# Kernel optimization log

Hardware: AMD Instinct MI355X
Metric: run time of the kernel (lower is better)

## Reference

```python
import jax, jax.numpy as jnp
import numpy as np

B, SEQ, DIM = 32, 512, 1024
DEPTH, HEADS, DHEAD = 6, 8, 64
INNER = HEADS * DHEAD  # 512
NLAT, MAXSEQ = 64, 512
EPS = 1e-5


def setup_inputs() -> dict:
    key = jax.random.key(0)
    ks = jax.random.split(key, 8)
    return {
        "x": jax.random.normal(ks[0], (B, SEQ, DIM), dtype=jnp.float32),
        "attention_mask": jax.random.randint(ks[1], (B, SEQ), 0, 2, dtype=jnp.int32),
        "latents": jax.random.normal(ks[2], (NLAT, DIM), dtype=jnp.float32),
        "media_pos_emb": jax.random.normal(ks[3], (MAXSEQ, DIM), dtype=jnp.float32),
        "ln_media_g": jnp.ones((DEPTH, DIM), jnp.float32),
        "ln_media_b": jnp.zeros((DEPTH, DIM), jnp.float32),
        "ln_lat_g": jnp.ones((DEPTH, DIM), jnp.float32),
        "ln_lat_b": jnp.zeros((DEPTH, DIM), jnp.float32),
        "Wq": jax.random.normal(ks[4], (DEPTH, DIM, INNER), dtype=jnp.float32) * 0.02,
        "Wkv": jax.random.normal(ks[5], (DEPTH, DIM, 2 * INNER), dtype=jnp.float32) * 0.02,
        "Wout": jax.random.normal(ks[6], (DEPTH, INNER, DIM), dtype=jnp.float32) * 0.02,
        "final_g": jnp.ones((DIM,), jnp.float32),
        "final_b": jnp.zeros((DIM,), jnp.float32),
    }


def _layer_norm(x, g, b):
    mu = jnp.mean(x, axis=-1, keepdims=True)
    var = jnp.mean(jnp.square(x - mu), axis=-1, keepdims=True)
    return (x - mu) * jax.lax.rsqrt(var + EPS) * g + b


def _heads(t):
    # b n (h d) -> b h n d
    b, n, _ = t.shape
    return t.reshape(b, n, HEADS, DHEAD).transpose(0, 2, 1, 3)


def reference(x, attention_mask, latents, media_pos_emb, ln_media_g, ln_media_b,
              ln_lat_g, ln_lat_b, Wq, Wkv, Wout, final_g, final_b):
    b, seq, _ = x.shape
    x = x + media_pos_emb[None, :seq, :]
    lat = jnp.broadcast_to(latents[None], (b, NLAT, DIM))
    scale = DHEAD ** -0.5
    # key mask over [latents ++ media]: latent keys never masked; 1 == masked
    key_mask = jnp.concatenate(
        [jnp.zeros((b, NLAT), attention_mask.dtype), attention_mask], axis=1)
    masked = (key_mask == 1)[:, None, None, :]  # b 1 1 j
    for l in range(DEPTH):
        xm = _layer_norm(x, ln_media_g[l], ln_media_b[l])
        ln = _layer_norm(lat, ln_lat_g[l], ln_lat_b[l])
        q = _heads(ln @ Wq[l])                      # b h i d
        kv = jnp.concatenate([ln, xm], axis=1) @ Wkv[l]
        k, v = jnp.split(kv, 2, axis=-1)
        k, v = _heads(k), _heads(v)                 # b h j d
        sim = jnp.einsum('bhid,bhjd->bhij', q * scale, k)
        sim = jnp.where(masked, -jnp.inf, sim)
        attn = jax.nn.softmax(sim, axis=-1)
        out = jnp.einsum('bhij,bhjd->bhid', attn, v)
        out = out.transpose(0, 2, 1, 3).reshape(b, NLAT, INNER)
        lat = lat + out @ Wout[l]
    return _layer_norm(lat, final_g, final_b)
```

## Files before the change

kernel.cpp:

```cpp
#include <hip/hip_runtime.h>
#include <cstdint>


#define DEVINL __device__ __forceinline__

typedef __attribute__((ext_vector_type(8))) short short8_t;
typedef __attribute__((ext_vector_type(4))) float f32x4;

DEVINL ushort f2bf(float f) {
  union { float f; uint32_t u; } c; c.f = f;
  uint32_t u = c.u;
  u += ((u >> 16) & 1u) + 0x7fffu;
  return (ushort)(u >> 16);
}
DEVINL float bf2f(ushort u) {
  union { uint32_t u; float f; } c; c.u = ((uint32_t)u) << 16;
  return c.f;
}
DEVINL f32x4 mfma16(short8_t a, short8_t b, f32x4 c) {
  return __builtin_amdgcn_mfma_f32_16x16x32_bf16(a, b, c, 0, 0, 0);
}
DEVINL void gld16(ushort* lds, const ushort* g) {
  __builtin_amdgcn_global_load_lds(
      (const __attribute__((address_space(1))) void*)g,
      (__attribute__((address_space(3))) void*)lds, 16, 0, 0);
}

__global__ __launch_bounds__(512, 2) void k_gemm256m(const ushort* __restrict__ A,
    const ushort* __restrict__ Bt, const float* __restrict__ bias,
    ushort* __restrict__ Kb, ushort* __restrict__ Vt) {
  extern __shared__ char lds[];
  constexpr int K = 1024, NT = 16;
  int tid = threadIdx.x, lane = tid & 63, w = tid >> 6;
  int wm = w >> 2, wn = w & 3;
  int fr = lane & 15;
  int fkb = (lane >> 4) << 4;
  int xorv = (fr & 7) << 4;
  int bid = blockIdx.x;
  int xcd = bid & 7, ii = bid >> 3;
  int m0 = (xcd * 8 + (ii >> 2)) * 256;
  int n0 = (ii & 3) * 256;
  int srow = w * 8 + (lane >> 3);
  int sce = ((lane & 7) ^ (lane >> 3)) << 3;
  const ushort* Ag = A + (size_t)(m0 + srow) * K + sce;
  const ushort* Bg = Bt + (size_t)(n0 + srow) * K + sce;
  f32x4 acc[8][4] = {};

  auto stA = [&](int t, int h) {
    ushort* d = (ushort*)(lds + (t % 3) * 32768 + h * 16384 + w * 1024);
    const ushort* s = Ag + (size_t)(h * 128) * K + t * 64;
    gld16(d, s);
    gld16((ushort*)((char*)d + 8192), s + (size_t)64 * K);
  };
  auto stB = [&](int t, int h) {
    ushort* d = (ushort*)(lds + 98304 + (t & 1) * 32768 + h * 16384 + w * 1024);
    const ushort* s = Bg + (size_t)(h * 128) * K + t * 64;
    gld16(d, s);
    gld16((ushort*)((char*)d + 8192), s + (size_t)64 * K);
  };
  stA(0, 0); stA(0, 1); stB(0, 0); stB(0, 1); stA(1, 0); stA(1, 1);

#define PHASE(MQ, STAGE_STMT)                                                  \
  do {                                                                         \
    _Pragma("unroll") for (int m2 = 0; m2 < 2; ++m2)                           \
      _Pragma("unroll") for (int kh = 0; kh < 2; ++kh)                         \
        afr[m2][kh] = *(const short8_t*)(ab +                                  \
            ((wm * 128 + (MQ + m2) * 16 + fr) << 7) +                          \
            ((kh * 64 + fkb) ^ xorv));                                         \
    STAGE_STMT;                                                                \
    asm volatile("s_waitcnt lgkmcnt(0)" ::: "memory");                         \
    __builtin_amdgcn_s_setprio(1);                                             \
    _Pragma("unroll") for (int m2 = 0; m2 < 2; ++m2)                           \
      _Pragma("unroll") for (int nt = 0; nt < 4; ++nt)                         \
        _Pragma("unroll") for (int kh = 0; kh < 2; ++kh)                       \
          acc[MQ + m2][nt] = mfma16(afr[m2][kh], bfr[nt][kh], acc[MQ + m2][nt]); \
    __builtin_amdgcn_s_setprio(0);                                             \
    __builtin_amdgcn_s_barrier();                                              \
  } while (0)

  for (int t = 0; t < NT; ++t) {
    const char* ab = lds + (t % 3) * 32768;
    const char* bb = lds + 98304 + (t & 1) * 32768;
    short8_t bfr[4][2], afr[2][2];
    if (t + 1 < NT) asm volatile("s_waitcnt vmcnt(4)" ::: "memory");
    else            asm volatile("s_waitcnt vmcnt(0)" ::: "memory");
    __builtin_amdgcn_s_barrier();
#pragma unroll
    for (int nt = 0; nt < 4; ++nt)
#pragma unroll
      for (int kh = 0; kh < 2; ++kh)
        bfr[nt][kh] = *(const short8_t*)(bb +
            ((wn * 64 + nt * 16 + fr) << 7) + ((kh * 64 + fkb) ^ xorv));
    PHASE(0, { if (t + 1 < NT) stB(t + 1, 0); });
    PHASE(2, { if (t + 1 < NT) stB(t + 1, 1); });
    PHASE(4, { if (t + 2 < NT) stA(t + 2, 0); });
    PHASE(6, { if (t + 2 < NT) stA(t + 2, 1); });
  }
#undef PHASE

  __syncthreads();
  ushort* Cl = (ushort*)lds;
  constexpr int CLS = 264;
  for (int p = 0; p < 2; ++p) {
    if (p) __syncthreads();
    if (wm == p) {
#pragma unroll
      for (int mt = 0; mt < 8; ++mt)
#pragma unroll
        for (int nt = 0; nt < 4; ++nt)
#pragma unroll
          for (int r = 0; r < 4; ++r) {
            int rl = mt * 16 + ((lane >> 4) << 2) + r;
            int cl = wn * 64 + nt * 16 + (lane & 15);
            Cl[rl * CLS + cl] = f2bf(acc[mt][nt][r] + bias[n0 + cl]);
          }
    }
    __syncthreads();
    int rowg0 = m0 + p * 128;
    int b_ = rowg0 >> 9;
    int jbase = 64 + (rowg0 & 511);
    if (n0 < 512) {
#pragma unroll
      for (int q2 = 0; q2 < 8; ++q2) {
        int task = tid + q2 * 512;
        int rl = task >> 5, ck = task & 31;
        short8_t vv = *(const short8_t*)&Cl[rl * CLS + ck * 8];
        *(short8_t*)&Kb[((size_t)(b_ * 576 + jbase + rl) << 9) + n0 + ck * 8] = vv;
      }
    } else {
#pragma unroll
      for (int q2 = 0; q2 < 8; ++q2) {
        int task = tid + q2 * 512;
        int d = task >> 4, jg = task & 15;
        short8_t vv;
#pragma unroll
        for (int e = 0; e < 8; ++e) vv[e] = (short)Cl[(jg * 8 + e) * CLS + d];
        *(short8_t*)&Vt[((size_t)(b_ * 512 + (n0 - 512) + d)) * 576 +
                        jbase + jg * 8] = vv;
      }
    }
  }
}

__global__ __launch_bounds__(256) void k_fold_kv(const float* __restrict__ Wkv,
    const float* __restrict__ lnmg, const float* __restrict__ lnlg,
    ushort* __restrict__ wkvmT, ushort* __restrict__ wlatT) {
  __shared__ float tile[32][33];
  int l = blockIdx.z;
  const float* Wl = Wkv + (size_t)l * 1048576;
  int r0 = blockIdx.y * 32, c0 = blockIdx.x * 32;
  int tx = threadIdx.x & 31, ty = threadIdx.x >> 5;
#pragma unroll
  for (int i = 0; i < 4; ++i)
    tile[ty + i * 8][tx] = Wl[(size_t)(r0 + ty + i * 8) * 1024 + c0 + tx];
  __syncthreads();
#pragma unroll
  for (int i = 0; i < 4; ++i) {
    int jl = ty + i * 8;
    float wv = tile[tx][jl];
    int r = r0 + tx, c = c0 + jl;
    wkvmT[(size_t)l * 1048576 + (size_t)c * 1024 + r] = f2bf(wv * lnmg[l * 1024 + r]);
    wlatT[(size_t)l * 1572864 + (size_t)(512 + c) * 1024 + r] = f2bf(wv * lnlg[l * 1024 + r]);
  }
}

__global__ __launch_bounds__(256) void k_fold_q(const float* __restrict__ Wq,
    const float* __restrict__ lnlg, ushort* __restrict__ wlatT) {
  __shared__ float tile[32][33];
  int l = blockIdx.z;
  const float* Wl = Wq + (size_t)l * 524288;
  int r0 = blockIdx.y * 32, c0 = blockIdx.x * 32;
  int tx = threadIdx.x & 31, ty = threadIdx.x >> 5;
#pragma unroll
  for (int i = 0; i < 4; ++i)
    tile[ty + i * 8][tx] = Wl[(size_t)(r0 + ty + i * 8) * 512 + c0 + tx];
  __syncthreads();
#pragma unroll
  for (int i = 0; i < 4; ++i) {
    int jl = ty + i * 8;
    int r = r0 + tx, c = c0 + jl;
    wlatT[(size_t)l * 1572864 + (size_t)c * 1024 + r] =
        f2bf(tile[tx][jl] * lnlg[l * 1024 + r] * 0.125f);
  }
}

__global__ __launch_bounds__(256) void k_fold_out(const float* __restrict__ Wout,
    ushort* __restrict__ woutT) {
  __shared__ float tile[32][33];
  int l = blockIdx.z;
  const float* Wl = Wout + (size_t)l * 524288;
  int r0 = blockIdx.y * 32, c0 = blockIdx.x * 32;
  int tx = threadIdx.x & 31, ty = threadIdx.x >> 5;
#pragma unroll
  for (int i = 0; i < 4; ++i)
    tile[ty + i * 8][tx] = Wl[(size_t)(r0 + ty + i * 8) * 1024 + c0 + tx];
  __syncthreads();
#pragma unroll
  for (int i = 0; i < 4; ++i) {
    int jl = ty + i * 8;
    woutT[(size_t)l * 524288 + (size_t)(c0 + jl) * 512 + r0 + tx] = f2bf(tile[tx][jl]);
  }
}

__global__ __launch_bounds__(256) void k_bias(const float* __restrict__ Wkv,
    const float* __restrict__ Wq, const float* __restrict__ lnmb,
    const float* __restrict__ lnlb, float* __restrict__ bkvm,
    float* __restrict__ blat) {
  __shared__ float red[4][64];
  int l = blockIdx.y;
  int c0 = blockIdx.x * 64;
  int tx = threadIdx.x & 63, dg = threadIdx.x >> 6;
  const float* Wsrc; const float* bv; int ld; float scale = 1.0f; float* outp;
  if (c0 < 1024) {
    Wsrc = Wkv + (size_t)l * 1048576 + c0 + tx; bv = lnmb + l * 1024; ld = 1024;
    outp = bkvm + l * 1024 + c0 + tx;
  } else if (c0 < 1536) {
    Wsrc = Wq + (size_t)l * 524288 + (c0 - 1024) + tx; bv = lnlb + l * 1024; ld = 512;
    outp = blat + l * 1536 + (c0 - 1024) + tx; scale = 0.125f;
  } else {
    Wsrc = Wkv + (size_t)l * 1048576 + (c0 - 1536) + tx; bv = lnlb + l * 1024; ld = 1024;
    outp = blat + l * 1536 + 512 + (c0 - 1536) + tx;
  }
  float acc = 0.f;
  for (int d = dg * 256; d < dg * 256 + 256; ++d)
    acc += bv[d] * Wsrc[(size_t)d * ld];
  red[dg][tx] = acc;
  __syncthreads();
  if (dg == 0) *outp = (red[0][tx] + red[1][tx] + red[2][tx] + red[3][tx]) * scale;
}

__global__ __launch_bounds__(256) void k_rownorm(const float* __restrict__ in,
    const float* __restrict__ pos, ushort* __restrict__ out) {
  int row = blockIdx.x, t = threadIdx.x;
  float4 v = *(const float4*)(in + (size_t)row * 1024 + t * 4);
  if (pos) {
    float4 p = *(const float4*)(pos + (size_t)(row & 511) * 1024 + t * 4);
    v.x += p.x; v.y += p.y; v.z += p.z; v.w += p.w;
  }
  float s = v.x + v.y + v.z + v.w;
  float q = v.x * v.x + v.y * v.y + v.z * v.z + v.w * v.w;
#pragma unroll
  for (int off = 32; off; off >>= 1) { s += __shfl_xor(s, off); q += __shfl_xor(q, off); }
  __shared__ float rs[4], rq[4];
  if ((t & 63) == 0) { rs[t >> 6] = s; rq[t >> 6] = q; }
  __syncthreads();
  s = rs[0] + rs[1] + rs[2] + rs[3];
  q = rq[0] + rq[1] + rq[2] + rq[3];
  float mean = s * (1.0f / 1024.0f);
  float var = q * (1.0f / 1024.0f) - mean * mean;
  float rstd = rsqrtf(var + 1e-5f);
  ushort4 o;
  o.x = f2bf((v.x - mean) * rstd);
  o.y = f2bf((v.y - mean) * rstd);
  o.z = f2bf((v.z - mean) * rstd);
  o.w = f2bf((v.w - mean) * rstd);
  *(ushort4*)(out + (size_t)row * 1024 + t * 4) = o;
}

__global__ __launch_bounds__(256) void k_finalln(const float* __restrict__ in,
    const float* __restrict__ g, const float* __restrict__ b, float* __restrict__ out) {
  int row = blockIdx.x, t = threadIdx.x;
  float4 v = *(const float4*)(in + (size_t)row * 1024 + t * 4);
  float s = v.x + v.y + v.z + v.w;
  float q = v.x * v.x + v.y * v.y + v.z * v.z + v.w * v.w;
#pragma unroll
  for (int off = 32; off; off >>= 1) { s += __shfl_xor(s, off); q += __shfl_xor(q, off); }
  __shared__ float rs[4], rq[4];
  if ((t & 63) == 0) { rs[t >> 6] = s; rq[t >> 6] = q; }
  __syncthreads();
  s = rs[0] + rs[1] + rs[2] + rs[3];
  q = rq[0] + rq[1] + rq[2] + rq[3];
  float mean = s * (1.0f / 1024.0f);
  float var = q * (1.0f / 1024.0f) - mean * mean;
  float rstd = rsqrtf(var + 1e-5f);
  float4 g4 = *(const float4*)(g + t * 4);
  float4 b4 = *(const float4*)(b + t * 4);
  float4 o;
  o.x = (v.x - mean) * rstd * g4.x + b4.x;
  o.y = (v.y - mean) * rstd * g4.y + b4.y;
  o.z = (v.z - mean) * rstd * g4.z + b4.z;
  o.w = (v.w - mean) * rstd * g4.w + b4.w;
  *(float4*)(out + (size_t)row * 1024 + t * 4) = o;
}

__global__ __launch_bounds__(256) void k_latinit(const float* __restrict__ latents,
                                                 float* __restrict__ lat) {
  int row = blockIdx.x, t = threadIdx.x;
  *(float4*)(lat + (size_t)row * 1024 + t * 4) =
      *(const float4*)(latents + (size_t)(row & 63) * 1024 + t * 4);
}

template <int MODE>
__global__ __launch_bounds__(256) void k_gemm64(const ushort* __restrict__ A,
    const ushort* __restrict__ Bt, const float* __restrict__ bias,
    ushort* __restrict__ o0, ushort* __restrict__ o1, ushort* __restrict__ o2,
    float* __restrict__ of, int N, int K) {
  __shared__ ushort Al[2][64][32];
  __shared__ ushort Bl[2][64][32];
  __shared__ ushort Cl[64][72];
  int tid = threadIdx.x, lane = tid & 63, w = tid >> 6;
  int wr = w >> 1, wc = w & 1;
  int m0 = blockIdx.y * 64, n0 = blockIdx.x * 64;
  f32x4 acc[2][2] = {};
  const ushort* Ag = A + (size_t)(m0 + w * 16 + (lane >> 2)) * K + (lane & 3) * 8;
  const ushort* Bg = Bt + (size_t)(n0 + w * 16 + (lane >> 2)) * K + (lane & 3) * 8;
  int fr = lane & 15, fk = (lane >> 4) << 3;
  int nt = K >> 5;
  gld16(&Al[0][w * 16][0], Ag);
  gld16(&Bl[0][w * 16][0], Bg);
  __syncthreads();
  for (int t = 0; t < nt; ++t) {
    int cur = t & 1;
    if (t + 1 < nt) {
      int k0 = (t + 1) << 5;
      gld16(&Al[cur ^ 1][w * 16][0], Ag + k0);
      gld16(&Bl[cur ^ 1][w * 16][0], Bg + k0);
    }
    short8_t a[2], b[2];
#pragma unroll
    for (int mt = 0; mt < 2; ++mt)
      a[mt] = *(const short8_t*)&Al[cur][wr * 32 + mt * 16 + fr][fk];
#pragma unroll
    for (int nt2 = 0; nt2 < 2; ++nt2)
      b[nt2] = *(const short8_t*)&Bl[cur][wc * 32 + nt2 * 16 + fr][fk];
#pragma unroll
    for (int mt = 0; mt < 2; ++mt)
#pragma unroll
      for (int nt2 = 0; nt2 < 2; ++nt2)
        acc[mt][nt2] = mfma16(a[mt], b[nt2], acc[mt][nt2]);
    __syncthreads();
  }
  if constexpr (MODE == 3) {
    if (n0 >= 1024) {
#pragma unroll
      for (int mt = 0; mt < 2; ++mt)
#pragma unroll
        for (int nt2 = 0; nt2 < 2; ++nt2)
#pragma unroll
          for (int r = 0; r < 4; ++r) {
            int rl = wr * 32 + mt * 16 + ((lane >> 4) << 2) + r;
            int col = wc * 32 + nt2 * 16 + (lane & 15);
            Cl[rl][col] = f2bf(acc[mt][nt2][r] + bias[n0 + col]);
          }
      __syncthreads();
      int b_ = m0 >> 6;
#pragma unroll
      for (int q = 0; q < 2; ++q) {
        int task = tid + q * 256;
        int jg = task & 7, d = task >> 3;
        short8_t vv;
#pragma unroll
        for (int e = 0; e < 8; ++e) vv[e] = (short)Cl[jg * 8 + e][d];
        *(short8_t*)&o2[((size_t)(b_ * 512 + (n0 - 1024) + d)) * 576 + jg * 8] = vv;
      }
      return;
    }
  }
#pragma unroll
  for (int mt = 0; mt < 2; ++mt)
#pragma unroll
    for (int nt2 = 0; nt2 < 2; ++nt2)
#pragma unroll
      for (int r = 0; r < 4; ++r) {
        int row = m0 + wr * 32 + mt * 16 + ((lane >> 4) << 2) + r;
        int col = n0 + wc * 32 + nt2 * 16 + (lane & 15);
        float v = acc[mt][nt2][r] + (bias ? bias[col] : 0.0f);
        if constexpr (MODE == 3) {
          int b_ = row >> 6, ii = row & 63;
          if (col < 512) o0[(size_t)row * 512 + col] = f2bf(v);
          else           o1[(((size_t)(b_ * 576 + ii)) << 9) + (col - 512)] = f2bf(v);
        } else {
          of[(size_t)row * N + col] += v;
        }
      }
}

__global__ __launch_bounds__(256) void k_attn(const ushort* __restrict__ Q,
    const ushort* __restrict__ Kb, const ushort* __restrict__ Vt,
    const int* __restrict__ amask, ushort* __restrict__ AO) {
  __shared__ ushort sim[32][584];
  int blk = blockIdx.x;
  int half = blk & 1, h = (blk >> 1) & 7, b = blk >> 4;
  int tid = threadIdx.x, lane = tid & 63, w = tid >> 6;
  int wr = w >> 1, wc = w & 1;
  short8_t aq0, aq1;
  {
    int qi = half * 32 + wr * 16 + (lane & 15);
    const ushort* qp = Q + ((size_t)(b * 64 + qi) << 9) + h * 64 + ((lane >> 4) << 3);
    aq0 = *(const short8_t*)qp;
    aq1 = *(const short8_t*)(qp + 32);
  }
  const ushort* kbase = Kb + (((size_t)(b * 576)) << 9) + h * 64 + ((lane >> 4) << 3);
  for (int jt = 0; jt < 9; ++jt) {
#pragma unroll
    for (int c2 = 0; c2 < 2; ++c2) {
      int ct = wc * 2 + c2;
      const ushort* kp = kbase + (((size_t)(jt * 64 + ct * 16 + (lane & 15))) << 9);
      short8_t bk0 = *(const short8_t*)kp;
      short8_t bk1 = *(const short8_t*)(kp + 32);
      f32x4 acc = {};
      acc = mfma16(aq0, bk0, acc);
      acc = mfma16(aq1, bk1, acc);
#pragma unroll
      for (int r = 0; r < 4; ++r)
        sim[wr * 16 + ((lane >> 4) << 2) + r][jt * 64 + ct * 16 + (lane & 15)] =
            f2bf(acc[r]);
    }
  }
  __syncthreads();
  unsigned mbits = 0;
#pragma unroll
  for (int c = 1; c < 9; ++c)
    if (amask[b * 512 + (c - 1) * 64 + lane]) mbits |= (1u << c);
  for (int rr = 0; rr < 8; ++rr) {
    int row = w * 8 + rr;
    float vals[9];
    float m = -3.0e38f;
#pragma unroll
    for (int c = 0; c < 9; ++c) {
      float v = bf2f(sim[row][c * 64 + lane]);
      vals[c] = v;
      if (!((mbits >> c) & 1)) m = fmaxf(m, v);
    }
#pragma unroll
    for (int off = 32; off; off >>= 1) m = fmaxf(m, __shfl_xor(m, off));
    float ssum = 0.f;
    float p[9];
#pragma unroll
    for (int c = 0; c < 9; ++c) {
      p[c] = ((mbits >> c) & 1) ? 0.f : __expf(vals[c] - m);
      ssum += p[c];
    }
#pragma unroll
    for (int off = 32; off; off >>= 1) ssum += __shfl_xor(ssum, off);
    float inv = 1.0f / ssum;
#pragma unroll
    for (int c = 0; c < 9; ++c)
      sim[row][c * 64 + lane] = f2bf(p[c] * inv);
  }
  __syncthreads();
  f32x4 oacc[2] = {};
  const ushort* vbase = Vt + ((size_t)(b * 512 + h * 64)) * 576 + ((lane >> 4) << 3);
  for (int jt = 0; jt < 9; ++jt) {
    short8_t pa0 = *(const short8_t*)&sim[wr * 16 + (lane & 15)][jt * 64 + ((lane >> 4) << 3)];
    short8_t pa1 = *(const short8_t*)&sim[wr * 16 + (lane & 15)][jt * 64 + 32 + ((lane >> 4) << 3)];
#pragma unroll
    for (int d2 = 0; d2 < 2; ++d2) {
      int dt = wc * 2 + d2;
      const ushort* vp = vbase + (size_t)(dt * 16 + (lane & 15)) * 576 + jt * 64;
      short8_t bv0 = *(const short8_t*)vp;
      short8_t bv1 = *(const short8_t*)(vp + 32);
      oacc[d2] = mfma16(pa0, bv0, oacc[d2]);
      oacc[d2] = mfma16(pa1, bv1, oacc[d2]);
    }
  }
#pragma unroll
  for (int d2 = 0; d2 < 2; ++d2) {
    int dt = wc * 2 + d2;
#pragma unroll
    for (int r = 0; r < 4; ++r) {
      int i = half * 32 + wr * 16 + ((lane >> 4) << 2) + r;
      int d = dt * 16 + (lane & 15);
      AO[((size_t)(b * 64 + i) << 9) + h * 64 + d] = f2bf(oacc[d2][r]);
    }
  }
}

extern "C" void kernel_launch(void* const* d_in, const int* in_sizes, int n_in,
                              void* d_out, int out_size, void* d_ws, size_t ws_size,
                              hipStream_t stream) {
  const float* x       = (const float*)d_in[0];
  const int*   amask   = (const int*)d_in[1];
  const float* latents = (const float*)d_in[2];
  const float* pos     = (const float*)d_in[3];
  const float* lnmg    = (const float*)d_in[4];
  const float* lnmb    = (const float*)d_in[5];
  const float* lnlg    = (const float*)d_in[6];
  const float* lnlb    = (const float*)d_in[7];
  const float* Wq      = (const float*)d_in[8];
  const float* Wkv     = (const float*)d_in[9];
  const float* Wout    = (const float*)d_in[10];
  const float* fg      = (const float*)d_in[11];
  const float* fb      = (const float*)d_in[12];
  float* out = (float*)d_out;
  char* ws = (char*)d_ws;

  ushort* xhat  = (ushort*)(ws + 0);
  ushort* wkvmT = (ushort*)(ws + 33554432);
  ushort* wlatT = (ushort*)(ws + 46137344);
  ushort* woutT = (ushort*)(ws + 65011712);
  float*  bkvm  = (float*)(ws + 71303168);
  float*  blat  = (float*)(ws + 71327744);
  float*  lat   = (float*)(ws + 71364608);
  ushort* lhat  = (ushort*)(ws + 79753216);
  ushort* qbuf  = (ushort*)(ws + 83947520);
  ushort* Kbuf  = (ushort*)(ws + 86044672);
  ushort* Vt    = (ushort*)(ws + 104919040);
  ushort* aobuf = (ushort*)(ws + 123793408);

  (void)hipFuncSetAttribute((const void*)k_gemm256m,
                            hipFuncAttributeMaxDynamicSharedMemorySize, 163840);

  dim3 B256(256);
  k_fold_kv<<<dim3(32, 32, 6), B256, 0, stream>>>(Wkv, lnmg, lnlg, wkvmT, wlatT);
  k_fold_q<<<dim3(16, 32, 6), B256, 0, stream>>>(Wq, lnlg, wlatT);
  k_fold_out<<<dim3(32, 16, 6), B256, 0, stream>>>(Wout, woutT);
  k_bias<<<dim3(40, 6), B256, 0, stream>>>(Wkv, Wq, lnmb, lnlb, bkvm, blat);
  k_rownorm<<<16384, B256, 0, stream>>>(x, pos, xhat);
  k_latinit<<<2048, B256, 0, stream>>>(latents, lat);

  for (int l = 0; l < 6; ++l) {
    k_rownorm<<<2048, B256, 0, stream>>>(lat, nullptr, lhat);
    k_gemm64<3><<<dim3(24, 32), B256, 0, stream>>>(
        lhat, wlatT + (size_t)l * 1572864, blat + l * 1536,
        qbuf, Kbuf, Vt, nullptr, 1536, 1024);
    k_gemm256m<<<dim3(256), dim3(512), 163840, stream>>>(
        xhat, wkvmT + (size_t)l * 1048576, bkvm + l * 1024, Kbuf, Vt);
    k_attn<<<512, B256, 0, stream>>>(qbuf, Kbuf, Vt, amask, aobuf);
    k_gemm64<2><<<dim3(16, 32), B256, 0, stream>>>(
        aobuf, woutT + (size_t)l * 524288, nullptr,
        nullptr, nullptr, nullptr, lat, 1024, 512);
  }
  k_finalln<<<2048, B256, 0, stream>>>(lat, fg, fb, out);
}
```

Measured before the change: 723.7 us.

## Double-buffer A fragments in GEMM loop and fuse bias into weight folding

The 256-row GEMM main loop now reads the next A fragments from LDS into an alternate register buffer before issuing the MFMA cluster on the current ones, so LDS latency overlaps matrix math. The explicit per-phase LDS wait is dropped. Separately, the LayerNorm-bias projection is computed inside the weight fold kernels by looping each block over all rows of a column strip, removing the separate bias kernel launch. This costs more registers in the GEMM and much smaller grids for the fold kernels, which may underfill the GPU.

```diff
diff --git a/kernel.cpp b/kernel.cpp
--- a/kernel.cpp
+++ b/kernel.cpp
@@ -60,28 +60,25 @@
   };
   stA(0, 0); stA(0, 1); stB(0, 0); stB(0, 1); stA(1, 0); stA(1, 1);
 
-#define PHASE(MQ, STAGE_STMT)                                                  \
-  do {                                                                         \
-    _Pragma("unroll") for (int m2 = 0; m2 < 2; ++m2)                           \
-      _Pragma("unroll") for (int kh = 0; kh < 2; ++kh)                         \
-        afr[m2][kh] = *(const short8_t*)(ab +                                  \
-            ((wm * 128 + (MQ + m2) * 16 + fr) << 7) +                          \
-            ((kh * 64 + fkb) ^ xorv));                                         \
-    STAGE_STMT;                                                                \
-    asm volatile("s_waitcnt lgkmcnt(0)" ::: "memory");                         \
-    __builtin_amdgcn_s_setprio(1);                                             \
+#define RD_AFR(DST, MQ)                                                        \
+  _Pragma("unroll") for (int m2 = 0; m2 < 2; ++m2)                             \
+    _Pragma("unroll") for (int kh = 0; kh < 2; ++kh)                           \
+      DST[m2][kh] = *(const short8_t*)(ab +                                    \
+          ((wm * 128 + (MQ + m2) * 16 + fr) << 7) + ((kh * 64 + fkb) ^ xorv));
+
+#define CLUSTER(MQ, AFR)                                                       \
+  __builtin_amdgcn_s_setprio(1);                                               \
+  _Pragma("unroll") for (int kh = 0; kh < 2; ++kh)                             \
     _Pragma("unroll") for (int m2 = 0; m2 < 2; ++m2)                           \
       _Pragma("unroll") for (int nt = 0; nt < 4; ++nt)                         \
-        _Pragma("unroll") for (int kh = 0; kh < 2; ++kh)                       \
-          acc[MQ + m2][nt] = mfma16(afr[m2][kh], bfr[nt][kh], acc[MQ + m2][nt]); \
-    __builtin_amdgcn_s_setprio(0);                                             \
-    __builtin_amdgcn_s_barrier();                                              \
-  } while (0)
+        acc[MQ + m2][nt] = mfma16(AFR[m2][kh], bfr[nt][kh], acc[MQ + m2][nt]); \
+  __builtin_amdgcn_s_setprio(0);                                               \
+  __builtin_amdgcn_s_barrier();
 
   for (int t = 0; t < NT; ++t) {
     const char* ab = lds + (t % 3) * 32768;
     const char* bb = lds + 98304 + (t & 1) * 32768;
-    short8_t bfr[4][2], afr[2][2];
+    short8_t bfr[4][2], afrX[2][2], afrY[2][2];
     if (t + 1 < NT) asm volatile("s_waitcnt vmcnt(4)" ::: "memory");
     else            asm volatile("s_waitcnt vmcnt(0)" ::: "memory");
     __builtin_amdgcn_s_barrier();
@@ -91,12 +88,21 @@
       for (int kh = 0; kh < 2; ++kh)
         bfr[nt][kh] = *(const short8_t*)(bb +
             ((wn * 64 + nt * 16 + fr) << 7) + ((kh * 64 + fkb) ^ xorv));
-    PHASE(0, { if (t + 1 < NT) stB(t + 1, 0); });
-    PHASE(2, { if (t + 1 < NT) stB(t + 1, 1); });
-    PHASE(4, { if (t + 2 < NT) stA(t + 2, 0); });
-    PHASE(6, { if (t + 2 < NT) stA(t + 2, 1); });
-  }
-#undef PHASE
+    RD_AFR(afrX, 0);
+    if (t + 1 < NT) stB(t + 1, 0);
+    RD_AFR(afrY, 2);
+    CLUSTER(0, afrX);
+    if (t + 1 < NT) stB(t + 1, 1);
+    RD_AFR(afrX, 4);
+    CLUSTER(2, afrY);
+    if (t + 2 < NT) stA(t + 2, 0);
+    RD_AFR(afrY, 6);
+    CLUSTER(4, afrX);
+    if (t + 2 < NT) stA(t + 2, 1);
+    CLUSTER(6, afrY);
+  }
+#undef RD_AFR
+#undef CLUSTER
 
   __syncthreads();
   ushort* Cl = (ushort*)lds;
@@ -144,43 +150,90 @@
 
 __global__ __launch_bounds__(256) void k_fold_kv(const float* __restrict__ Wkv,
     const float* __restrict__ lnmg, const float* __restrict__ lnlg,
-    ushort* __restrict__ wkvmT, ushort* __restrict__ wlatT) {
+    const float* __restrict__ lnmb, const float* __restrict__ lnlb,
+    ushort* __restrict__ wkvmT, ushort* __restrict__ wlatT,
+    float* __restrict__ bkvm, float* __restrict__ blat) {
   __shared__ float tile[32][33];
-  int l = blockIdx.z;
+  __shared__ float pm[8][32], pl[8][32];
+  int l = blockIdx.y;
+  int c0 = blockIdx.x * 32;
   const float* Wl = Wkv + (size_t)l * 1048576;
-  int r0 = blockIdx.y * 32, c0 = blockIdx.x * 32;
   int tx = threadIdx.x & 31, ty = threadIdx.x >> 5;
-#pragma unroll
-  for (int i = 0; i < 4; ++i)
-    tile[ty + i * 8][tx] = Wl[(size_t)(r0 + ty + i * 8) * 1024 + c0 + tx];
-  __syncthreads();
-#pragma unroll
-  for (int i = 0; i < 4; ++i) {
-    int jl = ty + i * 8;
-    float wv = tile[tx][jl];
-    int r = r0 + tx, c = c0 + jl;
-    wkvmT[(size_t)l * 1048576 + (size_t)c * 1024 + r] = f2bf(wv * lnmg[l * 1024 + r]);
-    wlatT[(size_t)l * 1572864 + (size_t)(512 + c) * 1024 + r] = f2bf(wv * lnlg[l * 1024 + r]);
+  float am = 0.f, al = 0.f;
+  for (int rt = 0; rt < 32; ++rt) {
+    int r0 = rt * 32;
+    __syncthreads();
+#pragma unroll
+    for (int i = 0; i < 4; ++i)
+      tile[ty + i * 8][tx] = Wl[(size_t)(r0 + ty + i * 8) * 1024 + c0 + tx];
+    __syncthreads();
+#pragma unroll
+    for (int i = 0; i < 4; ++i) {
+      int r = ty * 4 + i;
+      float wv = tile[r][tx];
+      am += lnmb[l * 1024 + r0 + r] * wv;
+      al += lnlb[l * 1024 + r0 + r] * wv;
+    }
+#pragma unroll
+    for (int i = 0; i < 4; ++i) {
+      int c = ty + i * 8;
+      float wv = tile[tx][c];
+      int r = r0 + tx;
+      wkvmT[(size_t)l * 1048576 + (size_t)(c0 + c) * 1024 + r] =
+          f2bf(wv * lnmg[l * 1024 + r]);
+      wlatT[(size_t)l * 1572864 + (size_t)(512 + c0 + c) * 1024 + r] =
+          f2bf(wv * lnlg[l * 1024 + r]);
+    }
+  }
+  pm[ty][tx] = am; pl[ty][tx] = al;
+  __syncthreads();
+  if (ty == 0) {
+    float sm = 0.f, sl = 0.f;
+#pragma unroll
+    for (int k = 0; k < 8; ++k) { sm += pm[k][tx]; sl += pl[k][tx]; }
+    bkvm[l * 1024 + c0 + tx] = sm;
+    blat[l * 1536 + 512 + c0 + tx] = sl;
   }
 }
 
 __global__ __launch_bounds__(256) void k_fold_q(const float* __restrict__ Wq,
-    const float* __restrict__ lnlg, ushort* __restrict__ wlatT) {
+    const float* __restrict__ lnlg, const float* __restrict__ lnlb,
+    ushort* __restrict__ wlatT, float* __restrict__ blat) {
   __shared__ float tile[32][33];
-  int l = blockIdx.z;
+  __shared__ float pq[8][32];
+  int l = blockIdx.y;
+  int c0 = blockIdx.x * 32;
   const float* Wl = Wq + (size_t)l * 524288;
-  int r0 = blockIdx.y * 32, c0 = blockIdx.x * 32;
   int tx = threadIdx.x & 31, ty = threadIdx.x >> 5;
-#pragma unroll
-  for (int i = 0; i < 4; ++i)
-    tile[ty + i * 8][tx] = Wl[(size_t)(r0 + ty + i * 8) * 512 + c0 + tx];
-  __syncthreads();
-#pragma unroll
-  for (int i = 0; i < 4; ++i) {
-    int jl = ty + i * 8;
-    int r = r0 + tx, c = c0 + jl;
-    wlatT[(size_t)l * 1572864 + (size_t)c * 1024 + r] =
-        f2bf(tile[tx][jl] * lnlg[l * 1024 + r] * 0.125f);
+  float aq = 0.f;
+  for (int rt = 0; rt < 32; ++rt) {
+    int r0 = rt * 32;
+    __syncthreads();
+#pragma unroll
+    for (int i = 0; i < 4; ++i)
+      tile[ty + i * 8][tx] = Wl[(size_t)(r0 + ty + i * 8) * 512 + c0 + tx];
+    __syncthreads();
+#pragma unroll
+    for (int i = 0; i < 4; ++i) {
+      int r = ty * 4 + i;
+      aq += lnlb[l * 1024 + r0 + r] * tile[r][tx];
+    }
+#pragma unroll
+    for (int i = 0; i < 4; ++i) {
+      int c = ty + i * 8;
+      float wv = tile[tx][c];
+      int r = r0 + tx;
+      wlatT[(size_t)l * 1572864 + (size_t)(c0 + c) * 1024 + r] =
+          f2bf(wv * lnlg[l * 1024 + r] * 0.125f);
+    }
+  }
+  pq[ty][tx] = aq;
+  __syncthreads();
+  if (ty == 0) {
+    float s = 0.f;
+#pragma unroll
+    for (int k = 0; k < 8; ++k) s += pq[k][tx];
+    blat[l * 1536 + c0 + tx] = s * 0.125f;
   }
 }
 
@@ -200,33 +253,6 @@
     int jl = ty + i * 8;
     woutT[(size_t)l * 524288 + (size_t)(c0 + jl) * 512 + r0 + tx] = f2bf(tile[tx][jl]);
   }
-}
-
-__global__ __launch_bounds__(256) void k_bias(const float* __restrict__ Wkv,
-    const float* __restrict__ Wq, const float* __restrict__ lnmb,
-    const float* __restrict__ lnlb, float* __restrict__ bkvm,
-    float* __restrict__ blat) {
-  __shared__ float red[4][64];
-  int l = blockIdx.y;
-  int c0 = blockIdx.x * 64;
-  int tx = threadIdx.x & 63, dg = threadIdx.x >> 6;
-  const float* Wsrc; const float* bv; int ld; float scale = 1.0f; float* outp;
-  if (c0 < 1024) {
-    Wsrc = Wkv + (size_t)l * 1048576 + c0 + tx; bv = lnmb + l * 1024; ld = 1024;
-    outp = bkvm + l * 1024 + c0 + tx;
-  } else if (c0 < 1536) {
-    Wsrc = Wq + (size_t)l * 524288 + (c0 - 1024) + tx; bv = lnlb + l * 1024; ld = 512;
-    outp = blat + l * 1536 + (c0 - 1024) + tx; scale = 0.125f;
-  } else {
-    Wsrc = Wkv + (size_t)l * 1048576 + (c0 - 1536) + tx; bv = lnlb + l * 1024; ld = 1024;
-    outp = blat + l * 1536 + 512 + (c0 - 1536) + tx;
-  }
-  float acc = 0.f;
-  for (int d = dg * 256; d < dg * 256 + 256; ++d)
-    acc += bv[d] * Wsrc[(size_t)d * ld];
-  red[dg][tx] = acc;
-  __syncthreads();
-  if (dg == 0) *outp = (red[0][tx] + red[1][tx] + red[2][tx] + red[3][tx]) * scale;
 }
 
 __global__ __launch_bounds__(256) void k_rownorm(const float* __restrict__ in,
@@ -502,10 +528,10 @@
                             hipFuncAttributeMaxDynamicSharedMemorySize, 163840);
 
   dim3 B256(256);
-  k_fold_kv<<<dim3(32, 32, 6), B256, 0, stream>>>(Wkv, lnmg, lnlg, wkvmT, wlatT);
-  k_fold_q<<<dim3(16, 32, 6), B256, 0, stream>>>(Wq, lnlg, wlatT);
+  k_fold_kv<<<dim3(32, 6), B256, 0, stream>>>(Wkv, lnmg, lnlg, lnmb, lnlb,
+                                              wkvmT, wlatT, bkvm, blat);
+  k_fold_q<<<dim3(16, 6), B256, 0, stream>>>(Wq, lnlg, lnlb, wlatT, blat);
   k_fold_out<<<dim3(32, 16, 6), B256, 0, stream>>>(Wout, woutT);
-  k_bias<<<dim3(40, 6), B256, 0, stream>>>(Wkv, Wq, lnmb, lnlb, bkvm, blat);
   k_rownorm<<<16384, B256, 0, stream>>>(x, pos, xhat);
   k_latinit<<<2048, B256, 0, stream>>>(latents, lat);
 
```

After: 737.9 us. Within noise of the previous version (+2.0%).
